# Performance work log

Measured on AMD Instinct MI355X. Metric: run time of the kernel, lower is better.

The kernel has to match this reference:

```python
import jax, jax.numpy as jnp
import numpy as np


def _aggregate(x, w, k, pad):
    """Involution-style per-pixel local conv.
    x: [N, C, H, W]; w: [N, heads, wc, k*k, H, W] (stride=1, dilation=1, zero pad).
    Returns [N, heads, C, H, W].
    """
    N, C, H, W = x.shape
    heads, wc = w.shape[1], w.shape[2]
    G = C // wc  # channel groups sharing the same per-pixel weights (c % wc)
    xp = jnp.pad(x, ((0, 0), (0, 0), (pad, pad), (pad, pad)))
    # unfold: [N, C, k*k, H, W] via k*k static shifted slices (no dynamic indexing)
    patches = jnp.stack(
        [xp[:, :, i:i + H, j:j + W] for i in range(k) for j in range(k)], axis=2
    )
    p = patches.reshape(N, G, wc, k * k, H, W)
    # out[n, e, g, v, h, w] = sum_k w[n, e, v, k, h, w] * p[n, g, v, k, h, w]
    out = jnp.einsum('nevkhw,ngvkhw->negvhw', w, p)
    return out.reshape(N, heads, C, H, W)


def reference(x, weight1, weight2):
    out1 = _aggregate(x, weight1, 3, 1)  # 3x3 branch, pad=1
    out2 = _aggregate(x, weight2, 5, 2)  # 5x5 branch, pad=2
    # output layout [N, 2, heads, C, H, W] matching the CUDA index arithmetic
    return jnp.stack([out1, out2], axis=1)


def setup_inputs() -> dict:
    key = jax.random.key(0)
    k1, k2, k3 = jax.random.split(key, 3)
    N, C, H, W = 4, 256, 56, 56
    heads, wc = 1, 32
    x = jax.random.normal(k1, (N, C, H, W), dtype=jnp.float32)
    weight1 = jax.random.normal(k2, (N, heads, wc, 9, H, W), dtype=jnp.float32)
    weight2 = jax.random.normal(k3, (N, heads, wc, 25, H, W), dtype=jnp.float32)
    return {"x": x, "weight1": weight1, "weight2": weight2}
```

## Files before the change

kernel.cpp:

```cpp
#include <hip/hip_runtime.h>


#define N_  4
#define C_  256
#define H_  56
#define W_  56
#define HW_ 3136
#define WC_ 32

#define TILE    7
#define LROWS   11
#define NPL     8
#define LSTRIDE 68

__global__ __launch_bounds__(256) void lconv_kernel(
    const float* __restrict__ x,
    const float* __restrict__ w1,
    const float* __restrict__ w2,
    float* __restrict__ out)
{
    __shared__ float lds[NPL * LROWS * LSTRIDE];

    const int b    = blockIdx.x;
    const int v    = b & 31;
    const int n    = (b >> 5) & 3;
    const int tile = b >> 7;
    const int r0   = tile * TILE;
    const int nv   = n * WC_ + v;
    const int tid  = threadIdx.x;

    for (int idx = tid; idx < NPL * LROWS * 14; idx += 256) {
        const int c4 = idx % 14;
        const int t2 = idx / 14;
        const int lr = t2 % LROWS;
        const int pl = t2 / LROWS;
        const int gr = r0 - 2 + lr;
        float4 val = make_float4(0.f, 0.f, 0.f, 0.f);
        if (gr >= 0 && gr < H_) {
            const int ch = pl * WC_ + v;
            val = *(const float4*)(x + (size_t)(n * C_ + ch) * HW_ + gr * W_ + c4 * 4);
        }
        float* lp = &lds[(pl * LROWS + lr) * LSTRIDE + 4 * c4 + 2];
        *(float2*)(lp)     = make_float2(val.x, val.y);
        *(float2*)(lp + 2) = make_float2(val.z, val.w);
    }
    for (int idx = tid; idx < NPL * LROWS * 4; idx += 256) {
        const int k  = idx & 3;
        const int t2 = idx >> 2;
        const int lr = t2 % LROWS;
        const int pl = t2 / LROWS;
        const int slot = (k < 2) ? k : (56 + k);
        lds[(pl * LROWS + lr) * LSTRIDE + slot] = 0.f;
    }
    __syncthreads();

    if (tid >= 2 * TILE * 14) return;

    const int ghalf = (tid >= TILE * 14) ? 1 : 0;
    const int t     = tid - ghalf * TILE * 14;
    const int row   = t / 14;
    const int s     = t - row * 14;
    const int wb    = 4 * s;
    const int gb    = ghalf * 4;
    const int h     = r0 + row;
    const int hw    = h * W_ + wb;

    const float* w1t = w1 + (size_t)nv * 9  * HW_ + hw;
    const float* w2t = w2 + (size_t)nv * 25 * HW_ + hw;
    const int c0 = gb * WC_ + v;

    float a2[4][4];
    #pragma unroll
    for (int g = 0; g < 4; ++g)
        #pragma unroll
        for (int p = 0; p < 4; ++p) a2[g][p] = 0.f;

    float4 w2cur[5], w2nxt[5];
    #pragma unroll
    for (int dj = 0; dj < 5; ++dj)
        w2cur[dj] = *(const float4*)(w2t + (size_t)dj * HW_);

    #pragma unroll 1
    for (int di = 0; di < 5; ++di) {
        if (di < 4) {
            #pragma unroll
            for (int dj = 0; dj < 5; ++dj)
                w2nxt[dj] = *(const float4*)(w2t + (size_t)((di + 1) * 5 + dj) * HW_);
        }
        #pragma unroll
        for (int g = 0; g < 4; ++g) {
            const float* lp = &lds[((gb + g) * LROWS + row + di) * LSTRIDE + wb];
            const float4 xa  = *(const float4*)(lp);
            const float4 xb4 = *(const float4*)(lp + 4);
            const float xw[8] = {xa.x, xa.y, xa.z, xa.w, xb4.x, xb4.y, xb4.z, xb4.w};
            #pragma unroll
            for (int dj = 0; dj < 5; ++dj) {
                const float* wr = (const float*)&w2cur[dj];
                #pragma unroll
                for (int p = 0; p < 4; ++p)
                    a2[g][p] += wr[p] * xw[p + dj];
            }
        }
        if (di < 4) {
            #pragma unroll
            for (int dj = 0; dj < 5; ++dj) w2cur[dj] = w2nxt[dj];
        }
    }

    float* o2 = out + ((size_t)(n * 2 + 1) * C_ + c0) * HW_ + hw;
    #pragma unroll
    for (int g = 0; g < 4; ++g)
        *(float4*)(o2 + (size_t)g * WC_ * HW_) =
            make_float4(a2[g][0], a2[g][1], a2[g][2], a2[g][3]);

    float a1[4][4];
    #pragma unroll
    for (int g = 0; g < 4; ++g)
        #pragma unroll
        for (int p = 0; p < 4; ++p) a1[g][p] = 0.f;

    float4 w1cur[3], w1nxt[3];
    #pragma unroll
    for (int dj = 0; dj < 3; ++dj)
        w1cur[dj] = *(const float4*)(w1t + (size_t)dj * HW_);

    #pragma unroll 1
    for (int di = 0; di < 3; ++di) {
        if (di < 2) {
            #pragma unroll
            for (int dj = 0; dj < 3; ++dj)
                w1nxt[dj] = *(const float4*)(w1t + (size_t)((di + 1) * 3 + dj) * HW_);
        }
        #pragma unroll
        for (int g = 0; g < 4; ++g) {
            const float* lp = &lds[((gb + g) * LROWS + row + 1 + di) * LSTRIDE + wb];
            const float4 xa  = *(const float4*)(lp);
            const float4 xb4 = *(const float4*)(lp + 4);
            const float xw[8] = {xa.x, xa.y, xa.z, xa.w, xb4.x, xb4.y, xb4.z, xb4.w};
            #pragma unroll
            for (int dj = 0; dj < 3; ++dj) {
                const float* wr = (const float*)&w1cur[dj];
                #pragma unroll
                for (int p = 0; p < 4; ++p)
                    a1[g][p] += wr[p] * xw[p + dj + 1];
            }
        }
        if (di < 2) {
            #pragma unroll
            for (int dj = 0; dj < 3; ++dj) w1cur[dj] = w1nxt[dj];
        }
    }

    float* o1 = out + ((size_t)(n * 2 + 0) * C_ + c0) * HW_ + hw;
    #pragma unroll
    for (int g = 0; g < 4; ++g)
        *(float4*)(o1 + (size_t)g * WC_ * HW_) =
            make_float4(a1[g][0], a1[g][1], a1[g][2], a1[g][3]);
}

extern "C" void kernel_launch(void* const* d_in, const int* in_sizes, int n_in,
                              void* d_out, int out_size, void* d_ws, size_t ws_size,
                              hipStream_t stream) {
    const float* x  = (const float*)d_in[0];
    const float* w1 = (const float*)d_in[1];
    const float* w2 = (const float*)d_in[2];
    float* out = (float*)d_out;

    dim3 grid(1024), block(256);
    hipLaunchKernelGGL(lconv_kernel, grid, block, 0, stream, x, w1, w2, out);
}
```

Measured before the change: 115.2 us.

## Shrink row tile, split channel groups across threads, fuse 3x3 and 5x5 loops

Reduces the row tile from 7 to 4, which raises the grid from 1024 to 1792 blocks. Each thread now handles 2 channel groups instead of 4, giving 224 active threads per block instead of 196. The 3x3 accumulation is folded into the 5x5 row loop so the same LDS reads of x serve both branches. The goal is more parallelism and less LDS traffic, at the cost of more halo reloads of x per output row and more weight refetches, because the weights are now loaded by 4 threads per pixel instead of 2.

```diff
diff --git a/kernel.cpp b/kernel.cpp
--- a/kernel.cpp
+++ b/kernel.cpp
@@ -8,8 +8,8 @@
 #define HW_ 3136
 #define WC_ 32
 
-#define TILE    7
-#define LROWS   11
+#define TILE    4
+#define LROWS   8
 #define NPL     8
 #define LSTRIDE 68
 
@@ -44,9 +44,9 @@
         *(float2*)(lp)     = make_float2(val.x, val.y);
         *(float2*)(lp + 2) = make_float2(val.z, val.w);
     }
-    for (int idx = tid; idx < NPL * LROWS * 4; idx += 256) {
-        const int k  = idx & 3;
-        const int t2 = idx >> 2;
+    {
+        const int k  = tid & 3;
+        const int t2 = tid >> 2;
         const int lr = t2 % LROWS;
         const int pl = t2 / LROWS;
         const int slot = (k < 2) ? k : (56 + k);
@@ -54,31 +54,32 @@
     }
     __syncthreads();
 
-    if (tid >= 2 * TILE * 14) return;
+    if (tid >= 224) return;
 
-    const int ghalf = (tid >= TILE * 14) ? 1 : 0;
-    const int t     = tid - ghalf * TILE * 14;
-    const int row   = t / 14;
-    const int s     = t - row * 14;
-    const int wb    = 4 * s;
-    const int gb    = ghalf * 4;
-    const int h     = r0 + row;
-    const int hw    = h * W_ + wb;
+    const int gq  = tid / 56;
+    const int r   = tid - gq * 56;
+    const int row = r / 14;
+    const int s   = r - row * 14;
+    const int wb  = 4 * s;
+    const int h   = r0 + row;
+    const int hw  = h * W_ + wb;
 
     const float* w1t = w1 + (size_t)nv * 9  * HW_ + hw;
     const float* w2t = w2 + (size_t)nv * 25 * HW_ + hw;
-    const int c0 = gb * WC_ + v;
 
-    float a2[4][4];
+    float a2[2][4], a1[2][4];
     #pragma unroll
-    for (int g = 0; g < 4; ++g)
+    for (int gi = 0; gi < 2; ++gi)
         #pragma unroll
-        for (int p = 0; p < 4; ++p) a2[g][p] = 0.f;
+        for (int p = 0; p < 4; ++p) { a2[gi][p] = 0.f; a1[gi][p] = 0.f; }
 
-    float4 w2cur[5], w2nxt[5];
+    float4 w2cur[5], w2nxt[5], w1cur[3], w1nxt[3];
     #pragma unroll
     for (int dj = 0; dj < 5; ++dj)
         w2cur[dj] = *(const float4*)(w2t + (size_t)dj * HW_);
+    #pragma unroll
+    for (int dj = 0; dj < 3; ++dj)
+        w1cur[dj] = *(const float4*)(w1t + (size_t)dj * HW_);
 
     #pragma unroll 1
     for (int di = 0; di < 5; ++di) {
@@ -87,9 +88,16 @@
             for (int dj = 0; dj < 5; ++dj)
                 w2nxt[dj] = *(const float4*)(w2t + (size_t)((di + 1) * 5 + dj) * HW_);
         }
+        if (di >= 1 && di < 3) {
+            #pragma unroll
+            for (int dj = 0; dj < 3; ++dj)
+                w1nxt[dj] = *(const float4*)(w1t + (size_t)(di * 3 + dj) * HW_);
+        }
+        const int do33 = (di >= 1 && di <= 3);
         #pragma unroll
-        for (int g = 0; g < 4; ++g) {
-            const float* lp = &lds[((gb + g) * LROWS + row + di) * LSTRIDE + wb];
+        for (int gi = 0; gi < 2; ++gi) {
+            const int g = gq + gi * 4;
+            const float* lp = &lds[(g * LROWS + row + di) * LSTRIDE + wb];
             const float4 xa  = *(const float4*)(lp);
             const float4 xb4 = *(const float4*)(lp + 4);
             const float xw[8] = {xa.x, xa.y, xa.z, xa.w, xb4.x, xb4.y, xb4.z, xb4.w};
@@ -98,64 +106,36 @@
                 const float* wr = (const float*)&w2cur[dj];
                 #pragma unroll
                 for (int p = 0; p < 4; ++p)
-                    a2[g][p] += wr[p] * xw[p + dj];
+                    a2[gi][p] += wr[p] * xw[p + dj];
+            }
+            if (do33) {
+                #pragma unroll
+                for (int dj = 0; dj < 3; ++dj) {
+                    const float* wr = (const float*)&w1cur[dj];
+                    #pragma unroll
+                    for (int p = 0; p < 4; ++p)
+                        a1[gi][p] += wr[p] * xw[p + dj + 1];
+                }
             }
         }
         if (di < 4) {
             #pragma unroll
             for (int dj = 0; dj < 5; ++dj) w2cur[dj] = w2nxt[dj];
         }
-    }
-
-    float* o2 = out + ((size_t)(n * 2 + 1) * C_ + c0) * HW_ + hw;
-    #pragma unroll
-    for (int g = 0; g < 4; ++g)
-        *(float4*)(o2 + (size_t)g * WC_ * HW_) =
-            make_float4(a2[g][0], a2[g][1], a2[g][2], a2[g][3]);
-
-    float a1[4][4];
-    #pragma unroll
-    for (int g = 0; g < 4; ++g)
-        #pragma unroll
-        for (int p = 0; p < 4; ++p) a1[g][p] = 0.f;
-
-    float4 w1cur[3], w1nxt[3];
-    #pragma unroll
-    for (int dj = 0; dj < 3; ++dj)
-        w1cur[dj] = *(const float4*)(w1t + (size_t)dj * HW_);
-
-    #pragma unroll 1
-    for (int di = 0; di < 3; ++di) {
-        if (di < 2) {
-            #pragma unroll
-            for (int dj = 0; dj < 3; ++dj)
-                w1nxt[dj] = *(const float4*)(w1t + (size_t)((di + 1) * 3 + dj) * HW_);
-        }
-        #pragma unroll
-        for (int g = 0; g < 4; ++g) {
-            const float* lp = &lds[((gb + g) * LROWS + row + 1 + di) * LSTRIDE + wb];
-            const float4 xa  = *(const float4*)(lp);
-            const float4 xb4 = *(const float4*)(lp + 4);
-            const float xw[8] = {xa.x, xa.y, xa.z, xa.w, xb4.x, xb4.y, xb4.z, xb4.w};
-            #pragma unroll
-            for (int dj = 0; dj < 3; ++dj) {
-                const float* wr = (const float*)&w1cur[dj];
-                #pragma unroll
-                for (int p = 0; p < 4; ++p)
-                    a1[g][p] += wr[p] * xw[p + dj + 1];
-            }
-        }
-        if (di < 2) {
+        if (di >= 1 && di < 3) {
             #pragma unroll
             for (int dj = 0; dj < 3; ++dj) w1cur[dj] = w1nxt[dj];
         }
     }
 
-    float* o1 = out + ((size_t)(n * 2 + 0) * C_ + c0) * HW_ + hw;
     #pragma unroll
-    for (int g = 0; g < 4; ++g)
-        *(float4*)(o1 + (size_t)g * WC_ * HW_) =
-            make_float4(a1[g][0], a1[g][1], a1[g][2], a1[g][3]);
+    for (int gi = 0; gi < 2; ++gi) {
+        const int ch = (gq + gi * 4) * WC_ + v;
+        float* o2 = out + ((size_t)(n * 2 + 1) * C_ + ch) * HW_ + hw;
+        float* o1 = out + ((size_t)(n * 2 + 0) * C_ + ch) * HW_ + hw;
+        *(float4*)(o2) = make_float4(a2[gi][0], a2[gi][1], a2[gi][2], a2[gi][3]);
+        *(float4*)(o1) = make_float4(a1[gi][0], a1[gi][1], a1[gi][2], a1[gi][3]);
+    }
 }
 
 extern "C" void kernel_launch(void* const* d_in, const int* in_sizes, int n_in,
@@ -166,6 +146,6 @@
     const float* w2 = (const float*)d_in[2];
     float* out = (float*)d_out;
 
-    dim3 grid(1024), block(256);
+    dim3 grid(1792), block(256);
     hipLaunchKernelGGL(lconv_kernel, grid, block, 0, stream, x, w1, w2, out);
 }
```

Measured after the change: 119.9 us. 1.04x slower.
